# Optimization experiments

Hardware: AMD Instinct MI355X
Metric: run time of the kernel (lower is better)

The kernel has to match this reference:

```python
import jax, jax.numpy as jnp
import numpy as np

# 8 shift directions (dh, dw): out[..., h, w] = x[..., h+dh, w+dw] (zero outside)
_OFFSETS = [(-1, 0), (1, 0), (0, -1), (0, 1), (-1, -1), (-1, 1), (1, -1), (1, 1)]


def setup_inputs() -> dict:
    key = jax.random.key(0)
    x = jax.random.normal(key, (32, 288, 64, 64), dtype=jnp.float32)
    return {"x": x}


def reference(x):
    B, C, H, W = x.shape
    cpg = C // 9  # channels_per_group = in_planes // kernel_size**2
    # zero-pad H and W by 1 so each shift is a single static slice of the pad
    xp = jnp.pad(x, ((0, 0), (0, 0), (1, 1), (1, 1)))
    groups = []
    for g, (dh, dw) in enumerate(_OFFSETS):
        groups.append(xp[:, g * cpg:(g + 1) * cpg, 1 + dh:1 + dh + H, 1 + dw:1 + dw + W])
    # group 8 (and any remainder channels) are never written in the original: stay zero
    rest = C - 8 * cpg
    if rest > 0:
        groups.append(jnp.zeros((B, rest, H, W), dtype=x.dtype))
    return jnp.concatenate(groups, axis=1)
```

## Files before the change

### kernel.cpp

```cpp
#include <hip/hip_runtime.h>


#define CC  288
#define HH  64
#define WW  64

typedef float v4f __attribute__((ext_vector_type(4)));

__global__ __launch_bounds__(256) void shift_kernel(const float* __restrict__ x,
                                                    float* __restrict__ out) {
    const int blk     = blockIdx.x;
    const int plane   = blk >> 2;
    const int quarter = blk & 3;
    const int c       = plane % CC;
    const int g       = c >> 5;

    const int t  = threadIdx.x;
    const int w0 = (t & 15) << 2;
    const int h  = (quarter << 4) + (t >> 4);

    v4f* dst = (v4f*)(out + (size_t)plane * (HH * WW) + h * WW + w0);

    if (g >= 8) {
        __builtin_nontemporal_store((v4f){0.f, 0.f, 0.f, 0.f}, dst);
        return;
    }

    const int dh = (int)((0x22001120u >> (g * 4)) & 0xFu) - 1;
    const int dw = (int)((0x20202011u >> (g * 4)) & 0xFu) - 1;

    const int hs = h + dh;
    if ((unsigned)hs >= (unsigned)HH) {
        __builtin_nontemporal_store((v4f){0.f, 0.f, 0.f, 0.f}, dst);
        return;
    }

    const float* __restrict__ row = x + (size_t)plane * (HH * WW) + hs * WW;

    v4f a = __builtin_nontemporal_load((const v4f*)(row + w0));

    v4f v;
    const int lane = t & 63;
    if (dw == 0) {
        v = a;
    } else if (dw == 1) {
        float nx = __shfl(a.x, lane + 1);
        v.x = a.y; v.y = a.z; v.z = a.w;
        v.w = (w0 == 60) ? 0.f : nx;
    } else {
        float pw = __shfl(a.w, lane - 1);
        v.x = (w0 == 0) ? 0.f : pw;
        v.y = a.x; v.z = a.y; v.w = a.z;
    }
    __builtin_nontemporal_store(v, dst);
}

extern "C" void kernel_launch(void* const* d_in, const int* in_sizes, int n_in,
                              void* d_out, int out_size, void* d_ws, size_t ws_size,
                              hipStream_t stream) {
    const float* x = (const float*)d_in[0];
    float* out = (float*)d_out;
    shift_kernel<<<dim3(32 * CC * 4), dim3(256), 0, stream>>>(x, out);
}
```

Baseline: 238.9 us.

## Use persistent grid-stride blocks with software-pipelined load of next tile

Replaces the one-block-per-quarter-plane launch with a fixed grid of 2048 blocks that stride over all tiles. Each iteration issues the load for the next tile before shuffling and storing the current one. The aim is to keep more loads in flight per wave and cut block launch overhead in this bandwidth-bound copy. In exchange it loses the early exit for zero tiles, and it may lose occupancy-based latency hiding compared with launching many blocks.

```diff
diff --git a/kernel.cpp b/kernel.cpp
--- a/kernel.cpp
+++ b/kernel.cpp
@@ -4,55 +4,67 @@
 #define CC  288
 #define HH  64
 #define WW  64
+#define NB  (32 * CC * 4)
+#define GRID 2048
 
 typedef float v4f __attribute__((ext_vector_type(4)));
 
 __global__ __launch_bounds__(256) void shift_kernel(const float* __restrict__ x,
                                                     float* __restrict__ out) {
-    const int blk     = blockIdx.x;
-    const int plane   = blk >> 2;
-    const int quarter = blk & 3;
-    const int c       = plane % CC;
-    const int g       = c >> 5;
+    const int t    = threadIdx.x;
+    const int w0   = (t & 15) << 2;
+    const int rr   = t >> 4;
+    const int lane = t & 63;
 
-    const int t  = threadIdx.x;
-    const int w0 = (t & 15) << 2;
-    const int h  = (quarter << 4) + (t >> 4);
+    auto stage = [&](int b, v4f& A, int& DW, float*& D) {
+        const int plane   = b >> 2;
+        const int quarter = b & 3;
+        const int c       = plane % CC;
+        const int g       = c >> 5;
+        const int h       = (quarter << 4) + rr;
+        D = out + (size_t)plane * (HH * WW) + h * WW + w0;
+        if (g >= 8) {
+            A = (v4f){0.f, 0.f, 0.f, 0.f};
+            DW = 0;
+            return;
+        }
+        const int dh = (int)((0x22001120u >> (g * 4)) & 0xFu) - 1;
+        DW           = (int)((0x20202011u >> (g * 4)) & 0xFu) - 1;
+        const int hs = h + dh;
+        if ((unsigned)hs >= (unsigned)HH) {
+            A = (v4f){0.f, 0.f, 0.f, 0.f};
+            return;
+        }
+        A = __builtin_nontemporal_load(
+                (const v4f*)(x + (size_t)plane * (HH * WW) + hs * WW + w0));
+    };
 
-    v4f* dst = (v4f*)(out + (size_t)plane * (HH * WW) + h * WW + w0);
+    auto process = [&](v4f A, int DW, float* D) {
+        v4f v;
+        if (DW == 0) {
+            v = A;
+        } else if (DW == 1) {
+            float nx = __shfl(A.x, (lane + 1) & 63);
+            v.x = A.y; v.y = A.z; v.z = A.w;
+            v.w = (w0 == 60) ? 0.f : nx;
+        } else {
+            float pw = __shfl(A.w, (lane - 1) & 63);
+            v.x = (w0 == 0) ? 0.f : pw;
+            v.y = A.x; v.z = A.y; v.w = A.z;
+        }
+        __builtin_nontemporal_store(v, (v4f*)D);
+    };
 
-    if (g >= 8) {
-        __builtin_nontemporal_store((v4f){0.f, 0.f, 0.f, 0.f}, dst);
-        return;
+    int b = blockIdx.x;
+    v4f a0; int d0; float* p0;
+    stage(b, a0, d0, p0);
+    for (int nb = b + GRID; nb < NB; nb += GRID) {
+        v4f a1; int d1; float* p1;
+        stage(nb, a1, d1, p1);
+        process(a0, d0, p0);
+        a0 = a1; d0 = d1; p0 = p1;
     }
-
-    const int dh = (int)((0x22001120u >> (g * 4)) & 0xFu) - 1;
-    const int dw = (int)((0x20202011u >> (g * 4)) & 0xFu) - 1;
-
-    const int hs = h + dh;
-    if ((unsigned)hs >= (unsigned)HH) {
-        __builtin_nontemporal_store((v4f){0.f, 0.f, 0.f, 0.f}, dst);
-        return;
-    }
-
-    const float* __restrict__ row = x + (size_t)plane * (HH * WW) + hs * WW;
-
-    v4f a = __builtin_nontemporal_load((const v4f*)(row + w0));
-
-    v4f v;
-    const int lane = t & 63;
-    if (dw == 0) {
-        v = a;
-    } else if (dw == 1) {
-        float nx = __shfl(a.x, lane + 1);
-        v.x = a.y; v.y = a.z; v.z = a.w;
-        v.w = (w0 == 60) ? 0.f : nx;
-    } else {
-        float pw = __shfl(a.w, lane - 1);
-        v.x = (w0 == 0) ? 0.f : pw;
-        v.y = a.x; v.z = a.y; v.w = a.z;
-    }
-    __builtin_nontemporal_store(v, dst);
+    process(a0, d0, p0);
 }
 
 extern "C" void kernel_launch(void* const* d_in, const int* in_sizes, int n_in,
@@ -60,5 +72,5 @@
                               hipStream_t stream) {
     const float* x = (const float*)d_in[0];
     float* out = (float*)d_out;
-    shift_kernel<<<dim3(32 * CC * 4), dim3(256), 0, stream>>>(x, out);
+    shift_kernel<<<dim3(GRID), dim3(256), 0, stream>>>(x, out);
 }
```

Result: slower. 245.0 us (+2.5%).
